# Kernel tuning notes

Hardware: AMD Instinct MI355X
Metric: run time of the kernel (lower is better)

## Reference

```python
import jax, jax.numpy as jnp
import numpy as np

B, T, E, H = 2, 1024, 2048, 32
D = E // H
GROUP = (0.25, 0.25, 0.25, 0.25)
NEG = float(np.finfo(np.float32).min)


def quant_per_token(t, n_bits):
    # smoothquant-style: clamp(absmax, 1e-5) / qmax, per last-dim row
    qmax = 2 ** (n_bits - 1) - 1
    s = jnp.clip(jnp.abs(t).max(-1, keepdims=True), 1e-5, None) / qmax
    return jnp.round(t / s) * s


def w8a8_linear(x, W, b, quant_out=False):
    xq = quant_per_token(x, 8)           # per-token act quant
    Wq = quant_per_token(W, 8)           # per-output-channel weight quant (W: [out, in])
    y = xq @ Wq.T + b
    return quant_per_token(y, 8) if quant_out else y


def to_heads(x):
    # [B, T, E] -> [B*H, T, D]
    return x.reshape(B, T, H, D).transpose(0, 2, 1, 3).reshape(B * H, T, D)


def setup_inputs() -> dict:
    key = jax.random.key(0)
    ks = jax.random.split(key, 9)
    hidden_states = jax.random.normal(ks[0], (B, T, E), jnp.float32)
    causal = jnp.where(jnp.tril(jnp.ones((T, T), bool)), 0.0, NEG).astype(jnp.float32)
    attention_mask = jnp.broadcast_to(causal[None, None], (B, 1, T, T))
    w = 0.02
    return {
        'hidden_states': hidden_states,
        'attention_mask': attention_mask,
        'Wq': jax.random.normal(ks[1], (E, E), jnp.float32) * w,
        'bq': jax.random.normal(ks[2], (E,), jnp.float32) * w,
        'Wk': jax.random.normal(ks[3], (E, E), jnp.float32) * w,
        'bk': jax.random.normal(ks[4], (E,), jnp.float32) * w,
        'Wv': jax.random.normal(ks[5], (E, E), jnp.float32) * w,
        'bv': jax.random.normal(ks[6], (E,), jnp.float32) * w,
        'Wo': jax.random.normal(ks[7], (E, E), jnp.float32) * w,
        'bo': jax.random.normal(ks[8], (E,), jnp.float32) * w,
    }


def reference(hidden_states, attention_mask, Wq, bq, Wk, bk, Wv, bv, Wo, bo):
    scaling = D ** -0.5
    q = w8a8_linear(hidden_states, Wq, bq, quant_out=True) * scaling  # [B,T,E]
    k = w8a8_linear(hidden_states, Wk, bk)                            # [B,T,E]
    v = w8a8_linear(hidden_states, Wv, bv)                            # [B,T,E]

    # ---- heavy-hitter scoring pass (pre-4bit-quant K) ----
    q1, k1 = to_heads(q), to_heads(k)                                 # [BH,T,D]
    aw = jnp.einsum('btd,bsd->bts', q1, k1)                           # [BH,T,T]
    aw = aw.reshape(B, H, T, T) + attention_mask
    aw = jnp.maximum(aw, NEG).reshape(B * H, T, T)
    tmp_attn = jax.nn.softmax(aw, axis=-1)
    acc = tmp_attn.sum(axis=1).sum(axis=0)[None, :]                   # [1,T]
    row_vector = jnp.arange(T, 0, -1).astype(jnp.float32)[None, :]    # T, T-1, ..., 1
    acc = acc / row_vector / (B * H)

    # ---- group-wise top-k heavy-hitter selection ----
    range_size_or = int(T / len(GROUP) / 2)
    start = 1
    idx_list = []
    for i, ratio in enumerate(GROUP):
        rs = int(T * ratio)
        end = min(start + rs - 1, T) if i < len(GROUP) - 1 else T
        partial = acc[:, start - 1:end]
        _, ti = jax.lax.top_k(partial, range_size_or)
        idx_list.append(ti + start - 1)
        start = end + 1
    topk_idx = jnp.concatenate(idx_list, axis=-1).reshape(-1)

    # ---- mixed-precision K quantization ----
    k_abs = jnp.abs(k)
    # fake_quant_mix (8-bit): amax(...)[0] in torch indexes batch 0 -> scales [T,1]
    s_mix = jnp.clip(k_abs.max(-1, keepdims=True)[0] / 127.0, 1e-5, None)  # [T,1]
    k_imp = jnp.round(k / s_mix) * s_mix
    # fake_quant (4-bit, per-row): clamp then divide by 7
    s4 = jnp.clip(k_abs.max(-1, keepdims=True), 1e-5, None) / 7.0
    kq = jnp.round(k / s4) * s4
    kq = kq.at[:, topk_idx, :].set(k_imp[:, topk_idx, :])
    # fake_quant_v (4-bit, per-tensor)
    sv = jnp.clip(jnp.abs(v).max(), 1e-5, None) / 7.0
    vq = jnp.round(v / sv) * sv

    # ---- actual attention with quantized K/V ----
    q2, k2, v2 = to_heads(q), to_heads(kq), to_heads(vq)
    aw2 = jnp.einsum('btd,bsd->bts', q2, k2).reshape(B, H, T, T) + attention_mask
    aw2 = jnp.maximum(aw2, NEG).reshape(B * H, T, T)
    probs = jax.nn.softmax(aw2, axis=-1)
    out = jnp.einsum('bts,bsd->btd', probs, v2)                       # [BH,T,D]
    out = out.reshape(B, H, T, D).transpose(0, 2, 1, 3).reshape(B, T, E)
    return w8a8_linear(out, Wo, bo)
```

## Files before the change

### kernel.cpp

```cpp
#include <hip/hip_runtime.h>
#include <stdint.h>

#define NEG_INF (-__builtin_inff())
#define L2E 1.4426950408889634f

namespace {
constexpr int kT   = 1024;
constexpr int kE   = 2048;
}

using bf16x8 = __attribute__((ext_vector_type(8))) short;
using f32x4  = __attribute__((ext_vector_type(4))) float;
using i32x4  = __attribute__((ext_vector_type(4))) int;
using i32x16 = __attribute__((ext_vector_type(16))) int;

#define MFMA_BF16(a, b, c) __builtin_amdgcn_mfma_f32_16x16x32_bf16((a), (b), (c), 0, 0, 0)
#define MFMA_I8_32(a, b, c) __builtin_amdgcn_mfma_i32_32x32x32_i8((a), (b), (c), 0, 0, 0)

__device__ __forceinline__ void gload16(const void* g, void* l) {
  __builtin_amdgcn_global_load_lds((const __attribute__((address_space(1))) unsigned*)g,
                                   (__attribute__((address_space(3))) unsigned*)l, 16, 0, 0);
}
__device__ __forceinline__ unsigned bfr(float x) {
  unsigned u = __float_as_uint(x);
  return (u + 0x7FFFu + ((u >> 16) & 1u)) >> 16;
}
__device__ __forceinline__ float bf2f(unsigned h) { return __uint_as_float(h << 16); }
__device__ __forceinline__ unsigned pk2(float a, float b) { return bfr(a) | (bfr(b) << 16); }
__device__ __forceinline__ float fexp2(float x) { return __builtin_amdgcn_exp2f(x); }

__device__ __forceinline__ float waveReduceMax(float v) {
#pragma unroll
  for (int o = 32; o > 0; o >>= 1) v = fmaxf(v, __shfl_down(v, o, 64));
  return v;
}
__device__ __forceinline__ float blockMax256(float v, float* r4) {
  const int tid = threadIdx.x;
  float wm = waveReduceMax(v);
  if ((tid & 63) == 0) r4[tid >> 6] = wm;
  __syncthreads();
  float bm = fmaxf(fmaxf(r4[0], r4[1]), fmaxf(r4[2], r4[3]));
  __syncthreads();
  return bm;
}

__global__ __launch_bounds__(256) void k_rowquant_all(const float* __restrict__ Xh,
                                                      const float* __restrict__ W0,
                                                      const float* __restrict__ W1,
                                                      const float* __restrict__ W2,
                                                      const float* __restrict__ W3,
                                                      int8_t* __restrict__ Qh,
                                                      int8_t* __restrict__ Q0,
                                                      int8_t* __restrict__ Q1,
                                                      int8_t* __restrict__ Q2,
                                                      int8_t* __restrict__ Q3,
                                                      float* __restrict__ sX,
                                                      float* __restrict__ sWall,
                                                      unsigned* __restrict__ vmax) {
  const int y = blockIdx.y;
  const float* X = (y == 0) ? Xh : (y == 1) ? W0 : (y == 2) ? W1 : (y == 3) ? W2 : W3;
  int8_t* Qp = (y == 0) ? Qh : (y == 1) ? Q0 : (y == 2) ? Q1 : (y == 3) ? Q2 : Q3;
  const int row = blockIdx.x;
  const int tid = threadIdx.x;
  if (row == 0 && y == 0 && tid == 0) *vmax = 0u;
  const float* x = X + (size_t)row * kE;
  __shared__ float r4[4];
  float am = 0.f;
  float4 v[2];
#pragma unroll
  for (int it = 0; it < 2; ++it) {
    v[it] = *reinterpret_cast<const float4*>(x + (size_t)(it * 256 + tid) * 4);
    am = fmaxf(am, fmaxf(fmaxf(fabsf(v[it].x), fabsf(v[it].y)), fmaxf(fabsf(v[it].z), fabsf(v[it].w))));
  }
  const float bm = blockMax256(am, r4);
  const float s = fmaxf(bm, 1e-5f) / 127.f;
  int8_t* xq = Qp + (size_t)row * kE;
#pragma unroll
  for (int it = 0; it < 2; ++it) {
    const int i = (it * 256 + tid) * 4;
    char4 q;
    q.x = (char)(int)rintf(v[it].x / s);
    q.y = (char)(int)rintf(v[it].y / s);
    q.z = (char)(int)rintf(v[it].z / s);
    q.w = (char)(int)rintf(v[it].w / s);
    *reinterpret_cast<char4*>(xq + i) = q;
  }
  if (tid == 0) {
    if (y == 0) sX[row] = s;
    else sWall[(y - 1) * kE + row] = s;
  }
}

__global__ __launch_bounds__(256) void k_rowquant_i8(const float* __restrict__ X,
                                                     int8_t* __restrict__ Xq,
                                                     float* __restrict__ S) {
  const int row = blockIdx.x;
  const int tid = threadIdx.x;
  const float* x = X + (size_t)row * kE;
  __shared__ float r4[4];
  float am = 0.f;
  float4 v[2];
#pragma unroll
  for (int it = 0; it < 2; ++it) {
    v[it] = *reinterpret_cast<const float4*>(x + (size_t)(it * 256 + tid) * 4);
    am = fmaxf(am, fmaxf(fmaxf(fabsf(v[it].x), fabsf(v[it].y)), fmaxf(fabsf(v[it].z), fabsf(v[it].w))));
  }
  const float bm = blockMax256(am, r4);
  const float s = fmaxf(bm, 1e-5f) / 127.f;
  int8_t* xq = Xq + (size_t)row * kE;
#pragma unroll
  for (int it = 0; it < 2; ++it) {
    const int i = (it * 256 + tid) * 4;
    char4 q;
    q.x = (char)(int)rintf(v[it].x / s);
    q.y = (char)(int)rintf(v[it].y / s);
    q.z = (char)(int)rintf(v[it].z / s);
    q.w = (char)(int)rintf(v[it].w / s);
    *reinterpret_cast<char4*>(xq + i) = q;
  }
  if (tid == 0) S[row] = s;
}

__global__ __launch_bounds__(256) void k_prep(const float* __restrict__ Qb,
                                              const float* __restrict__ Kb,
                                              const float* __restrict__ Vb,
                                              short* __restrict__ qi,
                                              float* __restrict__ sqg,
                                              short* __restrict__ khi,
                                              short* __restrict__ klo,
                                              float* __restrict__ s4,
                                              float* __restrict__ smix,
                                              unsigned* __restrict__ vmax) {
  const int row = blockIdx.x;
  const int tid = threadIdx.x;
  __shared__ float r4[4];

  {
    const float* x = Qb + (size_t)row * kE;
    float am = 0.f;
    float4 v[2];
#pragma unroll
    for (int it = 0; it < 2; ++it) {
      v[it] = *reinterpret_cast<const float4*>(x + (size_t)(it * 256 + tid) * 4);
      am = fmaxf(am, fmaxf(fmaxf(fabsf(v[it].x), fabsf(v[it].y)), fmaxf(fabsf(v[it].z), fabsf(v[it].w))));
    }
    const float bm = blockMax256(am, r4);
    const float s = fmaxf(bm, 1e-5f) / 127.f;
#pragma unroll
    for (int it = 0; it < 2; ++it) {
      const int i = (it * 256 + tid) * 4;
      short4 q;
      q.x = (short)bfr(rintf(v[it].x / s));
      q.y = (short)bfr(rintf(v[it].y / s));
      q.z = (short)bfr(rintf(v[it].z / s));
      q.w = (short)bfr(rintf(v[it].w / s));
      *reinterpret_cast<short4*>(qi + (size_t)row * kE + i) = q;
    }
    if (tid == 0) sqg[row] = s * 0.125f;
  }

  {
    const float* x = Kb + (size_t)row * kE;
    float am = 0.f;
    float4 v[2];
#pragma unroll
    for (int it = 0; it < 2; ++it) {
      v[it] = *reinterpret_cast<const float4*>(x + (size_t)(it * 256 + tid) * 4);
      am = fmaxf(am, fmaxf(fmaxf(fabsf(v[it].x), fabsf(v[it].y)), fmaxf(fabsf(v[it].z), fabsf(v[it].w))));
    }
    const float bm = blockMax256(am, r4);
#pragma unroll
    for (int it = 0; it < 2; ++it) {
      const int i = (it * 256 + tid) * 4;
      short4 hh, ll;
      unsigned hb;
      hb = bfr(v[it].x); hh.x = (short)hb; ll.x = (short)bfr(v[it].x - bf2f(hb));
      hb = bfr(v[it].y); hh.y = (short)hb; ll.y = (short)bfr(v[it].y - bf2f(hb));
      hb = bfr(v[it].z); hh.z = (short)hb; ll.z = (short)bfr(v[it].z - bf2f(hb));
      hb = bfr(v[it].w); hh.w = (short)hb; ll.w = (short)bfr(v[it].w - bf2f(hb));
      *reinterpret_cast<short4*>(khi + (size_t)row * kE + i) = hh;
      *reinterpret_cast<short4*>(klo + (size_t)row * kE + i) = ll;
    }
    if (tid == 0) {
      s4[row] = fmaxf(bm, 1e-5f) / 7.f;
      if (row < kT) smix[row] = fmaxf(bm / 127.f, 1e-5f);
    }
  }

  {
    const float* x = Vb + (size_t)row * kE;
    float am = 0.f;
#pragma unroll
    for (int it = 0; it < 2; ++it) {
      const float4 v = *reinterpret_cast<const float4*>(x + (size_t)(it * 256 + tid) * 4);
      am = fmaxf(am, fmaxf(fmaxf(fabsf(v.x), fabsf(v.y)), fmaxf(fabsf(v.z), fabsf(v.w))));
    }
    const float bm = blockMax256(am, r4);
    if (tid == 0) atomicMax(vmax, __float_as_uint(bm));
  }
}

__global__ __launch_bounds__(256) void k_kvint(const float* __restrict__ Kb,
                                               const float* __restrict__ s4,
                                               const float* __restrict__ smix,
                                               const int* __restrict__ sel,
                                               short* __restrict__ ki,
                                               float* __restrict__ skg,
                                               const float* __restrict__ Vb,
                                               const unsigned* __restrict__ vmax,
                                               short* __restrict__ vt) {
  const int bid = blockIdx.x;
  const int tid = threadIdx.x;
  if (bid < 2048) {
    const int row = bid;
    const int t = row & (kT - 1);
    const float s = sel[t] ? smix[t] : s4[row];
    const float* x = Kb + (size_t)row * kE;
#pragma unroll
    for (int it = 0; it < 2; ++it) {
      const int i = (it * 256 + tid) * 4;
      const float4 v = *reinterpret_cast<const float4*>(x + i);
      short4 q;
      q.x = (short)bfr(rintf(v.x / s));
      q.y = (short)bfr(rintf(v.y / s));
      q.z = (short)bfr(rintf(v.z / s));
      q.w = (short)bfr(rintf(v.w / s));
      *reinterpret_cast<short4*>(ki + (size_t)row * kE + i) = q;
    }
    if (tid == 0) skg[row] = s;
  } else {
    const int t = bid - 2048;
    const int tt = t & 15, bh = t >> 4;
    const int b = bh >> 5, h = bh & 31;
    const float sv = fmaxf(__uint_as_float(*vmax), 1e-5f) / 7.f;
    __shared__ short tr[64][80];
#pragma unroll
    for (int i = 0; i < 4; ++i) {
      const int e = i * 256 + tid;
      const int tok = e >> 4, d4 = (e & 15) * 4;
      const float4 v = *reinterpret_cast<const float4*>(
          &Vb[(size_t)(b * kT + tt * 64 + tok) * kE + h * 64 + d4]);
      tr[d4 + 0][tok] = (short)bfr(rintf(v.x / sv));
      tr[d4 + 1][tok] = (short)bfr(rintf(v.y / sv));
      tr[d4 + 2][tok] = (short)bfr(rintf(v.z / sv));
      tr[d4 + 3][tok] = (short)bfr(rintf(v.w / sv));
    }
    __syncthreads();
#pragma unroll
    for (int i = 0; i < 2; ++i) {
      const int e = i * 256 + tid;
      const int d = e >> 3, u = e & 7;
      const bf16x8 row = *reinterpret_cast<const bf16x8*>(&tr[d][u * 8]);
      *reinterpret_cast<bf16x8*>(&vt[(size_t)(bh * 64 + d) * kT + tt * 64 + u * 8]) = row;
    }
  }
}

__device__ __forceinline__ void gemm_i8_body(int m0, int n0,
                                             const int8_t* __restrict__ A,
                                             const float* __restrict__ sa,
                                             const int8_t* __restrict__ Bw,
                                             const float* __restrict__ sw,
                                             const float* __restrict__ bias,
                                             float* __restrict__ Y,
                                             int8_t* AsBase, int8_t* BsBase) {
  const int tid = threadIdx.x;
  const int lane = tid & 63, w = tid >> 6;
  const int l31 = lane & 31, lh = lane >> 5;
  const int wm = (w >> 1) * 64, wn = (w & 1) * 64;

  const i32x16 zero16 = {0};
  i32x16 acc00 = zero16, acc01 = zero16, acc10 = zero16, acc11 = zero16;

  auto stage = [&](int buf, int k0) {
    int8_t* As = AsBase + buf * 8192;
    int8_t* Bs = BsBase + buf * 8192;
#pragma unroll
    for (int i = 0; i < 2; ++i) {
      const int s = i * 256 + tid;
      const int row = s >> 2, gp = s & 3;
      const int gs = gp ^ ((row >> 1) & 3);
      gload16(A + (size_t)(m0 + row) * kE + k0 + gs * 16, As + s * 16);
    }
#pragma unroll
    for (int i = 0; i < 2; ++i) {
      const int s = i * 256 + tid;
      const int row = s >> 2, gp = s & 3;
      const int gs = gp ^ ((row >> 1) & 3);
      gload16(Bw + (size_t)(n0 + row) * kE + k0 + gs * 16, Bs + s * 16);
    }
  };

  stage(0, 0);
  __syncthreads();
  int cur = 0;

  const int ar0 = wm + l31, ar1 = wm + 32 + l31;
  const int br0 = wn + l31, br1 = wn + 32 + l31;
  const int sa0 = (ar0 >> 1) & 3, sa1 = (ar1 >> 1) & 3;
  const int sb0 = (br0 >> 1) & 3, sb1 = (br1 >> 1) & 3;

  for (int k0 = 0; k0 < kE; k0 += 64) {
    if (k0 + 64 < kE) stage(cur ^ 1, k0 + 64);
    const int8_t* As = AsBase + cur * 8192;
    const int8_t* Bs = BsBase + cur * 8192;
#pragma unroll
    for (int j = 0; j < 2; ++j) {
      const int gn = lh + 2 * j;
      const i32x4 a0 = *reinterpret_cast<const i32x4*>(As + ((ar0 << 2) + (gn ^ sa0)) * 16);
      const i32x4 a1 = *reinterpret_cast<const i32x4*>(As + ((ar1 << 2) + (gn ^ sa1)) * 16);
      const i32x4 b0 = *reinterpret_cast<const i32x4*>(Bs + ((br0 << 2) + (gn ^ sb0)) * 16);
      const i32x4 b1 = *reinterpret_cast<const i32x4*>(Bs + ((br1 << 2) + (gn ^ sb1)) * 16);
      acc00 = MFMA_I8_32(a0, b0, acc00);
      acc01 = MFMA_I8_32(a0, b1, acc01);
      acc10 = MFMA_I8_32(a1, b0, acc10);
      acc11 = MFMA_I8_32(a1, b1, acc11);
    }
    __syncthreads();
    cur ^= 1;
  }

#pragma unroll
  for (int fn = 0; fn < 2; ++fn) {
    const int col = n0 + wn + fn * 32 + l31;
    const float swn = sw[col], bn = bias[col];
#pragma unroll
    for (int fm = 0; fm < 2; ++fm) {
      const i32x16 accv = (fm == 0) ? ((fn == 0) ? acc00 : acc01)
                                    : ((fn == 0) ? acc10 : acc11);
      const int r0 = m0 + wm + fm * 32 + 4 * lh;
#pragma unroll
      for (int reg = 0; reg < 16; ++reg) {
        const int row = r0 + (reg & 3) + 8 * (reg >> 2);
        Y[(size_t)row * kE + col] = (float)accv[reg] * sa[row] * swn + bn;
      }
    }
  }
}

__global__ __launch_bounds__(256) void k_gemm_i8(const int8_t* __restrict__ A,
                                                 const float* __restrict__ sa,
                                                 const int8_t* __restrict__ Bw,
                                                 const float* __restrict__ sw,
                                                 const float* __restrict__ bias,
                                                 float* __restrict__ Y) {
  __shared__ int8_t As[2 * 8192];
  __shared__ int8_t Bs[2 * 8192];
  const int linear = blockIdx.x + (blockIdx.y << 4);
  const int nid = (linear & 7) * 32 + (linear >> 3);
  const int x = nid & 15, y = nid >> 4;
  gemm_i8_body(y * 128, x * 128, A, sa, Bw, sw, bias, Y, As, Bs);
}

__global__ __launch_bounds__(256) void k_gemm_qkv(const int8_t* __restrict__ A,
                                                  const float* __restrict__ sa,
                                                  const int8_t* __restrict__ Wq,
                                                  const int8_t* __restrict__ Wk,
                                                  const int8_t* __restrict__ Wv,
                                                  const float* __restrict__ sWall,
                                                  const float* __restrict__ bq,
                                                  const float* __restrict__ bk,
                                                  const float* __restrict__ bv,
                                                  float* __restrict__ qb,
                                                  float* __restrict__ kb,
                                                  float* __restrict__ vb) {
  __shared__ int8_t As[2 * 8192];
  __shared__ int8_t Bs[2 * 8192];
  const int linear = blockIdx.x + (blockIdx.y << 4) + (blockIdx.z << 8);
  const int nid = (linear & 7) * 96 + (linear >> 3);
  const int x = nid & 15, y = (nid >> 4) & 15, z = nid >> 8;
  const int8_t* Bw = (z == 0) ? Wq : (z == 1) ? Wk : Wv;
  const float* sw = sWall + (size_t)z * kE;
  const float* bias = (z == 0) ? bq : (z == 1) ? bk : bv;
  float* Y = (z == 0) ? qb : (z == 1) ? kb : vb;
  gemm_i8_body(y * 128, x * 128, A, sa, Bw, sw, bias, Y, As, Bs);
}

__global__ __launch_bounds__(512) void k_attn1(const short* __restrict__ qi,
                                               const short* __restrict__ khi,
                                               const short* __restrict__ klo,
                                               const float* __restrict__ sqg,
                                               float* __restrict__ accPart) {
  const int linear = blockIdx.x + (blockIdx.y << 3);
  const int nid = ((linear & 7) << 6) | (linear >> 3);
  const int r1 = nid & 7, r2 = 15 - r1, bh = nid >> 3;
  const int b = bh >> 5, h = bh & 31;
  const int tid = threadIdx.x, lane = tid & 63, w = tid >> 6;
  const int g = lane >> 4, c16 = lane & 15;
  const int swz = c16 & 7;
  const int myT = w >> 2, wl = w & 3;
  const int myr = myT ? r2 : r1;

  __shared__ short qs[2][64 * 64];
  __shared__ short hbuf[2][64 * 64];
  __shared__ short lbuf[2][64 * 64];
  __shared__ float accT[2][1024];
  __shared__ float Arow[128], Crow[128];

  for (int i = tid; i < 2048; i += 512) ((float*)accT)[i] = 0.f;

  const int st8 = tid >> 3, su = tid & 7;
  {
    const int co = ((su ^ (st8 & 7)) << 3);
    gload16(qi + (size_t)(b * kT + r1 * 64 + st8) * kE + h * 64 + co, &qs[0][st8 * 64 + su * 8]);
    gload16(qi + (size_t)(b * kT + r2 * 64 + st8) * kE + h * 64 + co, &qs[1][st8 * 64 + su * 8]);
  }
  auto stage = [&](int buf, int kt) {
    const int tokb = b * kT + kt * 64;
    const size_t gsrc = (size_t)(tokb + st8) * kE + h * 64 + ((su ^ (st8 & 7)) << 3);
    gload16(khi + gsrc, &hbuf[buf][st8 * 64 + su * 8]);
    gload16(klo + gsrc, &lbuf[buf][st8 * 64 + su * 8]);
  };

  stage(0, 0);
  __syncthreads();

  const int qrow = wl * 16 + c16;
  const short* qsp = qs[myT];
  const bf16x8 qf0 = *reinterpret_cast<const bf16x8*>(&qsp[qrow * 64 + ((g ^ swz) << 3)]);
  const bf16x8 qf1 = *reinterpret_cast<const bf16x8*>(&qsp[qrow * 64 + (((4 + g) ^ swz) << 3)]);
  const float Ac = sqg[b * kT + myr * 64 + qrow] * L2E;

  float m = NEG_INF, l = 0.f;
  int cur = 0;

  for (int kt = 0; kt <= r2; ++kt) {
    if (kt < r2) stage(cur ^ 1, kt + 1);
    if (kt <= myr) {
      float p[4][4];
      float pm = NEG_INF;
#pragma unroll
      for (int f = 0; f < 4; ++f) {
        const int tokl = f * 16 + c16;
        const bf16x8 ah0 = *reinterpret_cast<const bf16x8*>(&hbuf[cur][tokl * 64 + ((g ^ swz) << 3)]);
        const bf16x8 ah1 = *reinterpret_cast<const bf16x8*>(&hbuf[cur][tokl * 64 + (((4 + g) ^ swz) << 3)]);
        const bf16x8 al0 = *reinterpret_cast<const bf16x8*>(&lbuf[cur][tokl * 64 + ((g ^ swz) << 3)]);
        const bf16x8 al1 = *reinterpret_cast<const bf16x8*>(&lbuf[cur][tokl * 64 + (((4 + g) ^ swz) << 3)]);
        f32x4 sf = {0.f, 0.f, 0.f, 0.f};
        sf = MFMA_BF16(ah0, qf0, sf);
        sf = MFMA_BF16(ah1, qf1, sf);
        sf = MFMA_BF16(al0, qf0, sf);
        sf = MFMA_BF16(al1, qf1, sf);
#pragma unroll
        for (int r = 0; r < 4; ++r) {
          const int tokd = f * 16 + g * 4 + r;
          float s2 = sf[r] * Ac;
          if (kt == myr && tokd > qrow) s2 = NEG_INF;
          p[f][r] = s2;
          pm = fmaxf(pm, s2);
        }
      }
      pm = fmaxf(pm, __shfl_xor(pm, 16));
      pm = fmaxf(pm, __shfl_xor(pm, 32));
      const bool upd = pm > m + 8.f;
      const float mn = upd ? fmaxf(m, pm) : m;
      const float fsc = fexp2(m - mn);
      float rs = 0.f;
#pragma unroll
      for (int f = 0; f < 4; ++f)
#pragma unroll
        for (int r = 0; r < 4; ++r) rs += fexp2(p[f][r] - mn);
      rs += __shfl_xor(rs, 16);
      rs += __shfl_xor(rs, 32);
      l = l * fsc + rs;
      m = mn;
    }
    __syncthreads();
    cur ^= 1;
  }

  if (g == 0) {
    Arow[myT * 64 + qrow] = Ac;
    Crow[myT * 64 + qrow] = -(m + __builtin_amdgcn_logf(l));
  }
  stage(0, 0);
  __syncthreads();

  bf16x8 qa0[4], qa1[4];
  float Ar[4][4], Cr[4][4];
#pragma unroll
  for (int f = 0; f < 4; ++f) {
    const int qr = f * 16 + c16;
    qa0[f] = *reinterpret_cast<const bf16x8*>(&qsp[qr * 64 + ((g ^ swz) << 3)]);
    qa1[f] = *reinterpret_cast<const bf16x8*>(&qsp[qr * 64 + (((4 + g) ^ swz) << 3)]);
#pragma unroll
    for (int r = 0; r < 4; ++r) {
      const int tokd = myT * 64 + f * 16 + g * 4 + r;
      Ar[f][r] = Arow[tokd];
      Cr[f][r] = Crow[tokd];
    }
  }

  const int ktokL = wl * 16 + c16;
  cur = 0;
  for (int kt = 0; kt <= r2; ++kt) {
    if (kt < r2) stage(cur ^ 1, kt + 1);
    if (kt <= myr) {
      const bf16x8 kh0 = *reinterpret_cast<const bf16x8*>(&hbuf[cur][ktokL * 64 + ((g ^ swz) << 3)]);
      const bf16x8 kh1 = *reinterpret_cast<const bf16x8*>(&hbuf[cur][ktokL * 64 + (((4 + g) ^ swz) << 3)]);
      const bf16x8 kl0 = *reinterpret_cast<const bf16x8*>(&lbuf[cur][ktokL * 64 + ((g ^ swz) << 3)]);
      const bf16x8 kl1 = *reinterpret_cast<const bf16x8*>(&lbuf[cur][ktokL * 64 + (((4 + g) ^ swz) << 3)]);
      float csum = 0.f;
      if (kt < myr) {
#pragma unroll
        for (int f = 0; f < 4; ++f) {
          f32x4 sf = {0.f, 0.f, 0.f, 0.f};
          sf = MFMA_BF16(qa0[f], kh0, sf);
          sf = MFMA_BF16(qa1[f], kh1, sf);
          sf = MFMA_BF16(qa0[f], kl0, sf);
          sf = MFMA_BF16(qa1[f], kl1, sf);
#pragma unroll
          for (int r = 0; r < 4; ++r) csum += fexp2(fmaf(sf[r], Ar[f][r], Cr[f][r]));
        }
      } else {
#pragma unroll
        for (int f = 0; f < 4; ++f) {
          f32x4 sf = {0.f, 0.f, 0.f, 0.f};
          sf = MFMA_BF16(qa0[f], kh0, sf);
          sf = MFMA_BF16(qa1[f], kh1, sf);
          sf = MFMA_BF16(qa0[f], kl0, sf);
          sf = MFMA_BF16(qa1[f], kl1, sf);
#pragma unroll
          for (int r = 0; r < 4; ++r) {
            const float v = fexp2(fmaf(sf[r], Ar[f][r], Cr[f][r]));
            if (ktokL <= (f * 16 + g * 4 + r)) csum += v;
          }
        }
      }
      csum += __shfl_xor(csum, 16);
      csum += __shfl_xor(csum, 32);
      if (g == 0) accT[myT][kt * 64 + ktokL] += csum;
    }
    __syncthreads();
    cur ^= 1;
  }

  for (int i = tid; i < 1024; i += 512)
    accPart[(size_t)(bh * 8 + r1) * 1024 + i] = accT[0][i] + accT[1][i];
}

__global__ __launch_bounds__(1024) void k_acctopk(const float* __restrict__ part,
                                                  int* __restrict__ sel) {
  const int t = threadIdx.x;
  const int i = t & 255;
  const int sub = t >> 8;
  const int j = blockIdx.x * 256 + i;
  float s = 0.f;
  const int p0 = sub * 128;
  for (int p = p0; p < p0 + 128; ++p) s += part[(size_t)p * 1024 + j];
  __shared__ float partial[4][256];
  __shared__ float v[256];
  partial[sub][i] = s;
  __syncthreads();
  if (sub == 0) {
    const float tot = ((partial[0][i] + partial[1][i]) + partial[2][i]) + partial[3][i];
    v[i] = tot / (float)(kT - j) / 64.f;
  }
  __syncthreads();
  if (sub == 0) {
    const float vi = v[i];
    int rank = 0;
    for (int jj = 0; jj < 256; ++jj) {
      const float vj = v[jj];
      rank += (vj > vi) || (vj == vi && jj < i);
    }
    sel[j] = (rank < 128) ? 1 : 0;
  }
}

__global__ __launch_bounds__(512) void k_attn2(const short* __restrict__ qi,
                                               const short* __restrict__ ki,
                                               const short* __restrict__ vt,
                                               const float* __restrict__ sqg,
                                               const float* __restrict__ skg,
                                               const unsigned* __restrict__ vmax,
                                               float* __restrict__ ctx) {
  const int linear = blockIdx.x + (blockIdx.y << 3);
  const int nid = ((linear & 7) << 6) | (linear >> 3);
  const int r1 = nid & 7, r2 = 15 - r1, bh = nid >> 3;
  const int b = bh >> 5, h = bh & 31;
  const int tid = threadIdx.x, lane = tid & 63, w = tid >> 6;
  const int g = lane >> 4, c16 = lane & 15;
  const int swz = c16 & 7;
  const int myT = w >> 2, wl = w & 3;
  const int myr = myT ? r2 : r1;
  const int wrow = wl * 16 + c16;

  __shared__ short kbuf[2][64 * 64];
  __shared__ short vbuf[2][64 * 64];
  __shared__ float skl[2][64];

  const int qtok = b * kT + myr * 64 + wrow;
  bf16x8 qf[2];
  qf[0] = *reinterpret_cast<const bf16x8*>(qi + (size_t)qtok * kE + h * 64 + g * 8);
  qf[1] = *reinterpret_cast<const bf16x8*>(qi + (size_t)qtok * kE + h * 64 + 32 + g * 8);
  const float sq2 = sqg[qtok] * L2E;
  const float sv = fmaxf(__uint_as_float(*vmax), 1e-5f) / 7.f;

  const int st8 = tid >> 3, su = tid & 7;
  auto stage = [&](int buf, int kt) {
    const int tokb = b * kT + kt * 64;
    gload16(ki + (size_t)(tokb + st8) * kE + h * 64 + ((su ^ (st8 & 7)) << 3),
            &kbuf[buf][st8 * 64 + su * 8]);
    gload16(vt + (size_t)(bh * 64 + st8) * kT + kt * 64 + ((su ^ (st8 & 7)) << 3),
            &vbuf[buf][st8 * 64 + su * 8]);
    if (tid < 64) skl[buf][tid] = skg[tokb + tid];
  };

  float m = NEG_INF, l = 0.f;
  f32x4 ot[4];
#pragma unroll
  for (int f = 0; f < 4; ++f) ot[f] = (f32x4){0.f, 0.f, 0.f, 0.f};

  stage(0, 0);
  __syncthreads();
  int cur = 0;

  const int srcLo = c16 | ((g & 1) << 5);
  const int srcHi = srcLo | 16;
  const bool selq = ((g >> 1) & 1) != 0;

  for (int kt = 0; kt <= r2; ++kt) {
    if (kt < r2) stage(cur ^ 1, kt + 1);
    if (kt <= myr) {
      f32x4 sf4[4];
#pragma unroll
      for (int f = 0; f < 4; ++f) {
        const int tokl = f * 16 + c16;
        const bf16x8 k0 = *reinterpret_cast<const bf16x8*>(&kbuf[cur][tokl * 64 + ((g ^ swz) << 3)]);
        const bf16x8 k1 = *reinterpret_cast<const bf16x8*>(&kbuf[cur][tokl * 64 + (((4 + g) ^ swz) << 3)]);
        f32x4 s = {0.f, 0.f, 0.f, 0.f};
        s = MFMA_BF16(k0, qf[0], s);
        s = MFMA_BF16(k1, qf[1], s);
        sf4[f] = s;
      }

      float p[4][4];
      float pm = NEG_INF;
#pragma unroll
      for (int f = 0; f < 4; ++f)
#pragma unroll
        for (int r = 0; r < 4; ++r) {
          const int tokd = f * 16 + g * 4 + r;
          float s2 = sf4[f][r] * skl[cur][tokd] * sq2;
          if (kt == myr && tokd > wrow) s2 = NEG_INF;
          p[f][r] = s2;
          pm = fmaxf(pm, s2);
        }
      pm = fmaxf(pm, __shfl_xor(pm, 16));
      pm = fmaxf(pm, __shfl_xor(pm, 32));
      const bool upd = pm > m + 8.f;
      const float mn = upd ? fmaxf(m, pm) : m;
      const float fsc = fexp2(m - mn);
      m = mn;
      float rs = 0.f;
#pragma unroll
      for (int f = 0; f < 4; ++f)
#pragma unroll
        for (int r = 0; r < 4; ++r) {
          const float e = fexp2(p[f][r] - mn);
          p[f][r] = e;
          rs += e;
        }
      rs += __shfl_xor(rs, 16);
      rs += __shfl_xor(rs, 32);
      l = l * fsc + rs;
      if (__any(upd)) {
#pragma unroll
        for (int f = 0; f < 4; ++f)
#pragma unroll
          for (int r = 0; r < 4; ++r) ot[f][r] *= fsc;
      }
#pragma unroll
      for (int c = 0; c < 2; ++c) {
        const unsigned q0a = pk2(p[2 * c][0], p[2 * c][1]);
        const unsigned q0b = pk2(p[2 * c][2], p[2 * c][3]);
        const unsigned q1a = pk2(p[2 * c + 1][0], p[2 * c + 1][1]);
        const unsigned q1b = pk2(p[2 * c + 1][2], p[2 * c + 1][3]);
        unsigned a0, a1;
        union { unsigned u[4]; bf16x8 v; } Bh;
        a0 = __shfl(q0a, srcLo); a1 = __shfl(q1a, srcLo); Bh.u[0] = selq ? a1 : a0;
        a0 = __shfl(q0b, srcLo); a1 = __shfl(q1b, srcLo); Bh.u[1] = selq ? a1 : a0;
        a0 = __shfl(q0a, srcHi); a1 = __shfl(q1a, srcHi); Bh.u[2] = selq ? a1 : a0;
        a0 = __shfl(q0b, srcHi); a1 = __shfl(q1b, srcHi); Bh.u[3] = selq ? a1 : a0;
#pragma unroll
        for (int fd = 0; fd < 4; ++fd) {
          const int d = fd * 16 + c16;
          const bf16x8 va = *reinterpret_cast<const bf16x8*>(
              &vbuf[cur][d * 64 + ((((c << 2) | g) ^ swz) << 3)]);
          ot[fd] = MFMA_BF16(va, Bh.v, ot[fd]);
        }
      }
    }
    __syncthreads();
    cur ^= 1;
  }

  const float il = sv / l;
#pragma unroll
  for (int fd = 0; fd < 4; ++fd) {
    float4 o;
    o.x = ot[fd][0] * il;
    o.y = ot[fd][1] * il;
    o.z = ot[fd][2] * il;
    o.w = ot[fd][3] * il;
    *reinterpret_cast<float4*>(&ctx[(size_t)qtok * kE + h * 64 + fd * 16 + g * 4]) = o;
  }
}

extern "C" void kernel_launch(void* const* d_in, const int* in_sizes, int n_in,
                              void* d_out, int out_size, void* d_ws, size_t ws_size,
                              hipStream_t stream) {
  (void)in_sizes; (void)n_in; (void)out_size; (void)ws_size;
  const float* hs = (const float*)d_in[0];
  const float* Wq = (const float*)d_in[2];
  const float* bq = (const float*)d_in[3];
  const float* Wk = (const float*)d_in[4];
  const float* bk = (const float*)d_in[5];
  const float* Wv = (const float*)d_in[6];
  const float* bv = (const float*)d_in[7];
  const float* Wo = (const float*)d_in[8];
  const float* bo = (const float*)d_in[9];
  float* out = (float*)d_out;

  char* p = (char*)d_ws;
  auto take = [&](size_t bytes) {
    char* r = p;
    p += (bytes + 255) & ~(size_t)255;
    return r;
  };
  float* qb  = (float*)take((size_t)2048 * 2048 * 4);
  float* kb  = (float*)take((size_t)2048 * 2048 * 4);
  float* vb  = (float*)take((size_t)2048 * 2048 * 4);
  float* ctx = (float*)take((size_t)2048 * 2048 * 4);
  short* qiB = (short*)take((size_t)2048 * 2048 * 2);
  int8_t* xq  = (int8_t*)take((size_t)2048 * 2048);
  int8_t* woq = (int8_t*)take((size_t)2048 * 2048);
  float* sX    = (float*)take(2048 * 4);
  float* sWall = (float*)take(4 * 2048 * 4);
  float* sC    = (float*)take(2048 * 4);
  float* s4v   = (float*)take(2048 * 4);
  float* smix  = (float*)take(1024 * 4);
  int*   sel   = (int*)take(1024 * 4);
  float* sqg   = (float*)take(2048 * 4);
  float* skg   = (float*)take(2048 * 4);
  unsigned* vmax = (unsigned*)take(256);

  short* khi = (short*)qb;
  short* klo = (short*)qb + (size_t)2048 * 2048;
  short* kint = khi;
  short* vtp  = klo;
  float* accPart = ctx;
  int8_t* wqq = (int8_t*)ctx + ((size_t)2 << 20);
  int8_t* wkq = (int8_t*)ctx + ((size_t)6 << 20);
  int8_t* wvq = (int8_t*)ctx + ((size_t)10 << 20);
  int8_t* cq = xq;

  k_rowquant_all<<<dim3(2048, 5), 256, 0, stream>>>(hs, Wq, Wk, Wv, Wo,
                                                    xq, wqq, wkq, wvq, woq,
                                                    sX, sWall, vmax);

  k_gemm_qkv<<<dim3(16, 16, 3), 256, 0, stream>>>(xq, sX, wqq, wkq, wvq, sWall,
                                                  bq, bk, bv, qb, kb, vb);

  k_prep<<<2048, 256, 0, stream>>>(qb, kb, vb, qiB, sqg, khi, klo, s4v, smix, vmax);

  k_attn1<<<dim3(8, 64), 512, 0, stream>>>(qiB, khi, klo, sqg, accPart);
  k_acctopk<<<4, 1024, 0, stream>>>(accPart, sel);

  k_kvint<<<3072, 256, 0, stream>>>(kb, s4v, smix, sel, kint, skg, vb, vmax, vtp);

  k_attn2<<<dim3(8, 64), 512, 0, stream>>>(qiB, kint, vtp, sqg, skg, vmax, ctx);

  k_rowquant_i8<<<2048, 256, 0, stream>>>(ctx, cq, sC);
  k_gemm_i8<<<dim3(16, 16), 256, 0, stream>>>(cq, sC, woq, sWall + 3 * 2048, bo, out);
}
```

Before: 216.1 us.

## Split attn1 work across twice as many waves with partial softmax stat merge

Doubles k_attn1 blocks from 512 to 1024 threads. Each wave now handles half of the 16-row fragments, and per-half online softmax max/sum values are merged through shared memory before the second pass. The per-half column accumulators are kept separately and summed at the end. This is meant to raise wave-level parallelism on a grid of only 512 blocks, at the cost of an extra barrier, more shared memory, and idle threads during staging since only the first 512 threads issue loads.

```diff
diff --git a/kernel.cpp b/kernel.cpp
--- a/kernel.cpp
+++ b/kernel.cpp
@@ -376,11 +376,11 @@
   gemm_i8_body(y * 128, x * 128, A, sa, Bw, sw, bias, Y, As, Bs);
 }
 
-__global__ __launch_bounds__(512) void k_attn1(const short* __restrict__ qi,
-                                               const short* __restrict__ khi,
-                                               const short* __restrict__ klo,
-                                               const float* __restrict__ sqg,
-                                               float* __restrict__ accPart) {
+__global__ __launch_bounds__(1024) void k_attn1(const short* __restrict__ qi,
+                                                const short* __restrict__ khi,
+                                                const short* __restrict__ klo,
+                                                const float* __restrict__ sqg,
+                                                float* __restrict__ accPart) {
   const int linear = blockIdx.x + (blockIdx.y << 3);
   const int nid = ((linear & 7) << 6) | (linear >> 3);
   const int r1 = nid & 7, r2 = 15 - r1, bh = nid >> 3;
@@ -388,28 +388,35 @@
   const int tid = threadIdx.x, lane = tid & 63, w = tid >> 6;
   const int g = lane >> 4, c16 = lane & 15;
   const int swz = c16 & 7;
-  const int myT = w >> 2, wl = w & 3;
+  const int myT = w >> 3;
+  const int wl = (w >> 1) & 3;
+  const int fh = w & 1;
   const int myr = myT ? r2 : r1;
 
   __shared__ short qs[2][64 * 64];
   __shared__ short hbuf[2][64 * 64];
   __shared__ short lbuf[2][64 * 64];
-  __shared__ float accT[2][1024];
+  __shared__ float accT[2][2][1024];
   __shared__ float Arow[128], Crow[128];
-
-  for (int i = tid; i < 2048; i += 512) ((float*)accT)[i] = 0.f;
+  __shared__ float mpart[2][2][64], lpart[2][2][64];
+
+  for (int i = tid; i < 4096; i += 1024) ((float*)accT)[i] = 0.f;
 
   const int st8 = tid >> 3, su = tid & 7;
   {
-    const int co = ((su ^ (st8 & 7)) << 3);
-    gload16(qi + (size_t)(b * kT + r1 * 64 + st8) * kE + h * 64 + co, &qs[0][st8 * 64 + su * 8]);
-    gload16(qi + (size_t)(b * kT + r2 * 64 + st8) * kE + h * 64 + co, &qs[1][st8 * 64 + su * 8]);
+    if (tid < 512) {
+      const int co = ((su ^ (st8 & 7)) << 3);
+      gload16(qi + (size_t)(b * kT + r1 * 64 + st8) * kE + h * 64 + co, &qs[0][st8 * 64 + su * 8]);
+      gload16(qi + (size_t)(b * kT + r2 * 64 + st8) * kE + h * 64 + co, &qs[1][st8 * 64 + su * 8]);
+    }
   }
   auto stage = [&](int buf, int kt) {
-    const int tokb = b * kT + kt * 64;
-    const size_t gsrc = (size_t)(tokb + st8) * kE + h * 64 + ((su ^ (st8 & 7)) << 3);
-    gload16(khi + gsrc, &hbuf[buf][st8 * 64 + su * 8]);
-    gload16(klo + gsrc, &lbuf[buf][st8 * 64 + su * 8]);
+    if (tid < 512) {
+      const int tokb = b * kT + kt * 64;
+      const size_t gsrc = (size_t)(tokb + st8) * kE + h * 64 + ((su ^ (st8 & 7)) << 3);
+      gload16(khi + gsrc, &hbuf[buf][st8 * 64 + su * 8]);
+      gload16(klo + gsrc, &lbuf[buf][st8 * 64 + su * 8]);
+    }
   };
 
   stage(0, 0);
@@ -427,10 +434,11 @@
   for (int kt = 0; kt <= r2; ++kt) {
     if (kt < r2) stage(cur ^ 1, kt + 1);
     if (kt <= myr) {
-      float p[4][4];
+      float p[2][4];
       float pm = NEG_INF;
 #pragma unroll
-      for (int f = 0; f < 4; ++f) {
+      for (int fi = 0; fi < 2; ++fi) {
+        const int f = 2 * fh + fi;
         const int tokl = f * 16 + c16;
         const bf16x8 ah0 = *reinterpret_cast<const bf16x8*>(&hbuf[cur][tokl * 64 + ((g ^ swz) << 3)]);
         const bf16x8 ah1 = *reinterpret_cast<const bf16x8*>(&hbuf[cur][tokl * 64 + (((4 + g) ^ swz) << 3)]);
@@ -446,7 +454,7 @@
           const int tokd = f * 16 + g * 4 + r;
           float s2 = sf[r] * Ac;
           if (kt == myr && tokd > qrow) s2 = NEG_INF;
-          p[f][r] = s2;
+          p[fi][r] = s2;
           pm = fmaxf(pm, s2);
         }
       }
@@ -457,9 +465,9 @@
       const float fsc = fexp2(m - mn);
       float rs = 0.f;
 #pragma unroll
-      for (int f = 0; f < 4; ++f)
-#pragma unroll
-        for (int r = 0; r < 4; ++r) rs += fexp2(p[f][r] - mn);
+      for (int fi = 0; fi < 2; ++fi)
+#pragma unroll
+        for (int r = 0; r < 4; ++r) rs += fexp2(p[fi][r] - mn);
       rs += __shfl_xor(rs, 16);
       rs += __shfl_xor(rs, 32);
       l = l * fsc + rs;
@@ -470,24 +478,37 @@
   }
 
   if (g == 0) {
-    Arow[myT * 64 + qrow] = Ac;
-    Crow[myT * 64 + qrow] = -(m + __builtin_amdgcn_logf(l));
+    mpart[myT][fh][qrow] = m;
+    lpart[myT][fh][qrow] = l;
   }
   stage(0, 0);
   __syncthreads();
 
-  bf16x8 qa0[4], qa1[4];
-  float Ar[4][4], Cr[4][4];
-#pragma unroll
-  for (int f = 0; f < 4; ++f) {
+  if (tid < 128) {
+    const int tile = tid >> 6, row = tid & 63;
+    const int rr = tile ? r2 : r1;
+    const float m0 = mpart[tile][0][row], l0 = lpart[tile][0][row];
+    const float m1 = mpart[tile][1][row], l1 = lpart[tile][1][row];
+    const float mm = fmaxf(m0, m1);
+    const float ll = l0 * fexp2(m0 - mm) + l1 * fexp2(m1 - mm);
+    Arow[tile * 64 + row] = sqg[b * kT + rr * 64 + row] * L2E;
+    Crow[tile * 64 + row] = -(mm + __builtin_amdgcn_logf(ll));
+  }
+  __syncthreads();
+
+  bf16x8 qa0[2], qa1[2];
+  float Ar[2][4], Cr[2][4];
+#pragma unroll
+  for (int fi = 0; fi < 2; ++fi) {
+    const int f = 2 * fh + fi;
     const int qr = f * 16 + c16;
-    qa0[f] = *reinterpret_cast<const bf16x8*>(&qsp[qr * 64 + ((g ^ swz) << 3)]);
-    qa1[f] = *reinterpret_cast<const bf16x8*>(&qsp[qr * 64 + (((4 + g) ^ swz) << 3)]);
+    qa0[fi] = *reinterpret_cast<const bf16x8*>(&qsp[qr * 64 + ((g ^ swz) << 3)]);
+    qa1[fi] = *reinterpret_cast<const bf16x8*>(&qsp[qr * 64 + (((4 + g) ^ swz) << 3)]);
 #pragma unroll
     for (int r = 0; r < 4; ++r) {
       const int tokd = myT * 64 + f * 16 + g * 4 + r;
-      Ar[f][r] = Arow[tokd];
-      Cr[f][r] = Crow[tokd];
+      Ar[fi][r] = Arow[tokd];
+      Cr[fi][r] = Crow[tokd];
     }
   }
 
@@ -503,40 +524,44 @@
       float csum = 0.f;
       if (kt < myr) {
 #pragma unroll
-        for (int f = 0; f < 4; ++f) {
+        for (int fi = 0; fi < 2; ++fi) {
           f32x4 sf = {0.f, 0.f, 0.f, 0.f};
-          sf = MFMA_BF16(qa0[f], kh0, sf);
-          sf = MFMA_BF16(qa1[f], kh1, sf);
-          sf = MFMA_BF16(qa0[f], kl0, sf);
-          sf = MFMA_BF16(qa1[f], kl1, sf);
-#pragma unroll
-          for (int r = 0; r < 4; ++r) csum += fexp2(fmaf(sf[r], Ar[f][r], Cr[f][r]));
+          sf = MFMA_BF16(qa0[fi], kh0, sf);
+          sf = MFMA_BF16(qa1[fi], kh1, sf);
+          sf = MFMA_BF16(qa0[fi], kl0, sf);
+          sf = MFMA_BF16(qa1[fi], kl1, sf);
+#pragma unroll
+          for (int r = 0; r < 4; ++r) csum += fexp2(fmaf(sf[r], Ar[fi][r], Cr[fi][r]));
         }
       } else {
 #pragma unroll
-        for (int f = 0; f < 4; ++f) {
+        for (int fi = 0; fi < 2; ++fi) {
+          const int f = 2 * fh + fi;
           f32x4 sf = {0.f, 0.f, 0.f, 0.f};
-          sf = MFMA_BF16(qa0[f], kh0, sf);
-          sf = MFMA_BF16(qa1[f], kh1, sf);
-          sf = MFMA_BF16(qa0[f], kl0, sf);
-          sf = MFMA_BF16(qa1[f], kl1, sf);
+          sf = MFMA_BF16(qa0[fi], kh0, sf);
+          sf = MFMA_BF16(qa1[fi], kh1, sf);
+          sf = MFMA_BF16(qa0[fi], kl0, sf);
+          sf = MFMA_BF16(qa1[fi], kl1, sf);
 #pragma unroll
           for (int r = 0; r < 4; ++r) {
-            const float v = fexp2(fmaf(sf[r], Ar[f][r], Cr[f][r]));
+            const float v = fexp2(fmaf(sf[r], Ar[fi][r], Cr[fi][r]));
             if (ktokL <= (f * 16 + g * 4 + r)) csum += v;
           }
         }
       }
       csum += __shfl_xor(csum, 16);
       csum += __shfl_xor(csum, 32);
-      if (g == 0) accT[myT][kt * 64 + ktokL] += csum;
+      if (g == 0) accT[myT][fh][kt * 64 + ktokL] += csum;
     }
     __syncthreads();
     cur ^= 1;
   }
 
-  for (int i = tid; i < 1024; i += 512)
-    accPart[(size_t)(bh * 8 + r1) * 1024 + i] = accT[0][i] + accT[1][i];
+  {
+    const int i = tid;
+    accPart[(size_t)(bh * 8 + r1) * 1024 + i] =
+        (accT[0][0][i] + accT[0][1][i]) + (accT[1][0][i] + accT[1][1][i]);
+  }
 }
 
 __global__ __launch_bounds__(1024) void k_acctopk(const float* __restrict__ part,
@@ -765,7 +790,7 @@
 
   k_prep<<<2048, 256, 0, stream>>>(qb, kb, vb, qiB, sqg, khi, klo, s4v, smix, vmax);
 
-  k_attn1<<<dim3(8, 64), 512, 0, stream>>>(qiB, khi, klo, sqg, accPart);
+  k_attn1<<<dim3(8, 64), 1024, 0, stream>>>(qiB, khi, klo, sqg, accPart);
   k_acctopk<<<4, 1024, 0, stream>>>(accPart, sel);
 
   k_kvint<<<3072, 256, 0, stream>>>(kb, s4v, smix, sel, kint, skg, vb, vmax, vtp);
```

Result: slower. 222.6 us (+3.0%).
